# Performance work log

Measured on AMD Instinct MI355X. Metric: run time of the kernel, lower is better.

The kernel has to match this reference:

```python
import jax, jax.numpy as jnp
import numpy as np

WINDOW_SIZE = 11
C1 = 0.01 ** 2
C2 = 0.03 ** 2


def _make_window(size: int) -> jnp.ndarray:
    sigma = size / 6.0
    coords = jnp.arange(size, dtype=jnp.float32) - size // 2
    g = jnp.exp(-coords ** 2 / (2 * sigma ** 2))
    g = g / g.sum()
    w = jnp.outer(g, g)
    return w[None, None]  # [1,1,K,K]  (OIHW)


def _conv(x, w, pad):
    # x: [N,1,H,W], w: [1,1,K,K]
    return jax.lax.conv_general_dilated(
        x, w,
        window_strides=(1, 1),
        padding=[(pad, pad), (pad, pad)],
        dimension_numbers=("NCHW", "OIHW", "NCHW"),
    )


def setup_inputs() -> dict:
    key = jax.random.key(0)
    k1, k2 = jax.random.split(key)
    pred = jax.random.uniform(k1, (64, 1, 512, 512), dtype=jnp.float32)
    gt = jax.random.uniform(k2, (64, 1, 512, 512), dtype=jnp.float32)
    return {"pred": pred, "gt": gt}


def reference(pred, gt):
    w = _make_window(WINDOW_SIZE).astype(pred.dtype)
    pad = WINDOW_SIZE // 2
    mu1 = _conv(pred, w, pad)
    mu2 = _conv(gt, w, pad)
    sigma1 = _conv(pred * pred, w, pad) - mu1 ** 2
    sigma2 = _conv(gt * gt, w, pad) - mu2 ** 2
    sigma12 = _conv(pred * gt, w, pad) - mu1 * mu2
    ssim_map = (2 * mu1 * mu2 + C1) * (2 * sigma12 + C2) / (
        (mu1 ** 2 + mu2 ** 2 + C1) * (sigma1 + sigma2 + C2)
    )
    return 1 - ssim_map.mean()
```

## Files before the change

### kernel.cpp

```cpp
#include <hip/hip_runtime.h>
#include <math.h>

#define IMG_H 512
#define IMG_W 512
#define NIMG 64
#define TH 64
#define TCOLS 256
#define HALO 5
#define KSIZE 11
#define LROW (TCOLS + 2*HALO)

__global__ __launch_bounds__(256, 4)
void ssim_main(const float* __restrict__ pred, const float* __restrict__ gt,
               float* __restrict__ partial) {
    __shared__ float sp[2][LROW];
    __shared__ float sg[2][LROW];
    __shared__ float wsum[4];

    const int tid = threadIdx.x;
    const int bid = blockIdx.x;
    const int img = bid >> 4;
    const int rem = bid & 15;
    const int c0  = (rem & 1) * TCOLS;
    const int r0  = (rem >> 1) * TH;

    float wgt[KSIZE];
    {
        const float sigma = 11.0f / 6.0f;
        float s = 0.f;
        #pragma unroll
        for (int i = 0; i < KSIZE; ++i) {
            float d = (float)(i - 5);
            wgt[i] = expf(-d * d / (2.f * sigma * sigma));
            s += wgt[i];
        }
        float inv = 1.f / s;
        #pragma unroll
        for (int i = 0; i < KSIZE; ++i) wgt[i] *= inv;
    }

    const float* pimg = pred + (size_t)img * IMG_H * IMG_W;
    const float* gimg = gt   + (size_t)img * IMG_H * IMG_W;

    const int  cs0   = c0 - HALO + tid;
    const int  cs1   = cs0 + 256;
    const bool has2  = tid < (LROW - 256);
    const bool c0ok  = (cs0 >= 0) && (cs0 < IMG_W);
    const bool c1ok  = has2 && (cs1 < IMG_W);

    float stp0, stp1, stg0, stg1;

    auto load_row = [&](int r, float& p0, float& p1, float& g0, float& g1) {
        const bool rok = (r >= 0) && (r < IMG_H);
        const float* prow = pimg + (size_t)r * IMG_W;
        const float* grow = gimg + (size_t)r * IMG_W;
        p0 = (rok && c0ok) ? prow[cs0] : 0.f;
        g0 = (rok && c0ok) ? grow[cs0] : 0.f;
        p1 = (rok && c1ok) ? prow[cs1] : 0.f;
        g1 = (rok && c1ok) ? grow[cs1] : 0.f;
    };

    const int r_in0 = r0 - HALO;
    load_row(r_in0, stp0, stp1, stg0, stg1);

    float rp[KSIZE], rg[KSIZE], rpp[KSIZE], rgg[KSIZE], rpg[KSIZE];
    float lsum = 0.f;

    const float C1 = 1e-4f;
    const float C2 = 9e-4f;

    #pragma unroll 1
    for (int ob = 0; ob < 7; ++ob) {
        #pragma unroll
        for (int jj = 0; jj < KSIZE; ++jj) {
            const int i   = ob * KSIZE + jj;
            const int r   = r_in0 + i;
            const int cur = i & 1;

            sp[cur][tid] = stp0;
            sg[cur][tid] = stg0;
            if (has2) { sp[cur][tid + 256] = stp1; sg[cur][tid + 256] = stg1; }

            load_row(r + 1, stp0, stp1, stg0, stg1);

            __syncthreads();

            float hp = 0.f, hg = 0.f, hpp = 0.f, hgg = 0.f, hpg = 0.f;
            #pragma unroll
            for (int k = 0; k < KSIZE; ++k) {
                float p  = sp[cur][tid + k];
                float g  = sg[cur][tid + k];
                float t1 = wgt[k] * p;
                float t2 = wgt[k] * g;
                hp += t1;
                hg += t2;
                hpp = fmaf(t1, p, hpp);
                hgg = fmaf(t2, g, hgg);
                hpg = fmaf(t1, g, hpg);
            }
            rp[jj] = hp; rg[jj] = hg; rpp[jj] = hpp; rgg[jj] = hgg; rpg[jj] = hpg;

            if (i >= 10 && i < 10 + TH) {
                float mu1 = 0.f, mu2 = 0.f, svpp = 0.f, svgg = 0.f, svpg = 0.f;
                #pragma unroll
                for (int d = 0; d < KSIZE; ++d) {
                    const int slot = (jj + 1 + d) % KSIZE;
                    const float wv = wgt[d];
                    mu1  = fmaf(wv, rp[slot],  mu1);
                    mu2  = fmaf(wv, rg[slot],  mu2);
                    svpp = fmaf(wv, rpp[slot], svpp);
                    svgg = fmaf(wv, rgg[slot], svgg);
                    svpg = fmaf(wv, rpg[slot], svpg);
                }
                const float m11 = mu1 * mu1;
                const float m22 = mu2 * mu2;
                const float m12 = mu1 * mu2;
                const float s1  = svpp - m11;
                const float s2  = svgg - m22;
                const float s12 = svpg - m12;
                const float num = fmaf(2.f, m12, C1) * fmaf(2.f, s12, C2);
                const float den = (m11 + m22 + C1) * (s1 + s2 + C2);
                lsum += num * __builtin_amdgcn_rcpf(den);
            }
        }
    }

    #pragma unroll
    for (int off = 32; off > 0; off >>= 1) lsum += __shfl_down(lsum, off);
    if ((tid & 63) == 0) wsum[tid >> 6] = lsum;
    __syncthreads();
    if (tid == 0) {
        float b = wsum[0] + wsum[1] + wsum[2] + wsum[3];
        atomicAdd(partial, b);
    }
}

__global__ void ssim_final(const float* __restrict__ partial,
                           float* __restrict__ out) {
    out[0] = 1.f - partial[0] * (1.f / (float)((size_t)NIMG * IMG_H * IMG_W));
}

extern "C" void kernel_launch(void* const* d_in, const int* in_sizes, int n_in,
                              void* d_out, int out_size, void* d_ws, size_t ws_size,
                              hipStream_t stream) {
    const float* pred = (const float*)d_in[0];
    const float* gt   = (const float*)d_in[1];
    float* out = (float*)d_out;
    float* ws  = (float*)d_ws;

    hipMemsetAsync(ws, 0, sizeof(float), stream);

    const int nblocks = NIMG * (IMG_W / TCOLS) * (IMG_H / TH);
    ssim_main<<<nblocks, 256, 0, stream>>>(pred, gt, ws);
    ssim_final<<<1, 1, 0, stream>>>(ws, out);
}
```

Measured before the change: 191.5 us.

## Give each wavefront its own 64-column strip to replace block barriers with wave barriers

Each of the four wavefronts now processes an independent 64-column strip with its own single-buffered shared-memory row of 74 floats. The per-row __syncthreads is replaced by wave-local barriers, removing block-wide synchronisation. The row loop is unrolled through templated step calls. In exchange, each strip reloads its 10-column halo, raising halo overhead from 10/256 to 10/64 per row, and loads narrow to 64-wide segments. It also adds a clamp so rows past the tile's last needed input are not loaded.

Measured after the change: 185.3 us. -3.3%, faster.

```diff
diff --git a/kernel.cpp b/kernel.cpp
--- a/kernel.cpp
+++ b/kernel.cpp
@@ -1,28 +1,30 @@
 #include <hip/hip_runtime.h>
 #include <math.h>
+#include <type_traits>
 
 #define IMG_H 512
 #define IMG_W 512
 #define NIMG 64
 #define TH 64
-#define TCOLS 256
 #define HALO 5
 #define KSIZE 11
-#define LROW (TCOLS + 2*HALO)
+#define LROW 74
 
 __global__ __launch_bounds__(256, 4)
 void ssim_main(const float* __restrict__ pred, const float* __restrict__ gt,
                float* __restrict__ partial) {
-    __shared__ float sp[2][LROW];
-    __shared__ float sg[2][LROW];
+    __shared__ float sp[4][LROW];
+    __shared__ float sg[4][LROW];
     __shared__ float wsum[4];
 
-    const int tid = threadIdx.x;
-    const int bid = blockIdx.x;
-    const int img = bid >> 4;
-    const int rem = bid & 15;
-    const int c0  = (rem & 1) * TCOLS;
-    const int r0  = (rem >> 1) * TH;
+    const int tid  = threadIdx.x;
+    const int wv   = tid >> 6;
+    const int lane = tid & 63;
+    const int bid  = blockIdx.x;
+    const int img  = bid >> 4;
+    const int rem  = bid & 15;
+    const int c0   = (rem & 1) * 256 + wv * 64;
+    const int r0   = (rem >> 1) * TH;
 
     float wgt[KSIZE];
     {
@@ -42,92 +44,106 @@
     const float* pimg = pred + (size_t)img * IMG_H * IMG_W;
     const float* gimg = gt   + (size_t)img * IMG_H * IMG_W;
 
-    const int  cs0   = c0 - HALO + tid;
-    const int  cs1   = cs0 + 256;
-    const bool has2  = tid < (LROW - 256);
-    const bool c0ok  = (cs0 >= 0) && (cs0 < IMG_W);
-    const bool c1ok  = has2 && (cs1 < IMG_W);
+    const int  cs0  = c0 - HALO + lane;
+    const int  cs1  = cs0 + 64;
+    const bool has2 = lane < (LROW - 64);
+    const bool c0ok = (cs0 >= 0) && (cs0 < IMG_W);
+    const bool c1ok = has2 && (cs1 < IMG_W);
+    const int  r_in0 = r0 - HALO;
+    const int  rtop  = r_in0 + 73;
 
     float stp0, stp1, stg0, stg1;
-
-    auto load_row = [&](int r, float& p0, float& p1, float& g0, float& g1) {
-        const bool rok = (r >= 0) && (r < IMG_H);
-        const float* prow = pimg + (size_t)r * IMG_W;
-        const float* grow = gimg + (size_t)r * IMG_W;
-        p0 = (rok && c0ok) ? prow[cs0] : 0.f;
-        g0 = (rok && c0ok) ? grow[cs0] : 0.f;
-        p1 = (rok && c1ok) ? prow[cs1] : 0.f;
-        g1 = (rok && c1ok) ? grow[cs1] : 0.f;
+    auto load_row = [&](int rr) {
+        const bool rok = (rr >= 0) && (rr < IMG_H) && (rr <= rtop);
+        const float* prow = pimg + (size_t)rr * IMG_W;
+        const float* grow = gimg + (size_t)rr * IMG_W;
+        stp0 = (rok && c0ok) ? prow[cs0] : 0.f;
+        stg0 = (rok && c0ok) ? grow[cs0] : 0.f;
+        stp1 = (rok && c1ok) ? prow[cs1] : 0.f;
+        stg1 = (rok && c1ok) ? grow[cs1] : 0.f;
     };
-
-    const int r_in0 = r0 - HALO;
-    load_row(r_in0, stp0, stp1, stg0, stg1);
+    load_row(r_in0);
 
     float rp[KSIZE], rg[KSIZE], rpp[KSIZE], rgg[KSIZE], rpg[KSIZE];
     float lsum = 0.f;
+    const float C1v = 1e-4f;
+    const float C2v = 9e-4f;
 
-    const float C1 = 1e-4f;
-    const float C2 = 9e-4f;
+    float* swp = &sp[wv][0];
+    float* swg = &sg[wv][0];
+
+    auto step = [&](int i, auto jc) {
+        constexpr int jj = decltype(jc)::value;
+        const int r = r_in0 + i;
+
+        __builtin_amdgcn_wave_barrier();
+
+        swp[lane] = stp0;
+        swg[lane] = stg0;
+        if (has2) { swp[lane + 64] = stp1; swg[lane + 64] = stg1; }
+
+        load_row(r + 1);
+
+        __builtin_amdgcn_wave_barrier();
+
+        float hp = 0.f, hg = 0.f, hpp = 0.f, hgg = 0.f, hpg = 0.f;
+        #pragma unroll
+        for (int k = 0; k < KSIZE; ++k) {
+            float p  = swp[lane + k];
+            float g  = swg[lane + k];
+            float t1 = wgt[k] * p;
+            float t2 = wgt[k] * g;
+            hp += t1;
+            hg += t2;
+            hpp = fmaf(t1, p, hpp);
+            hgg = fmaf(t2, g, hgg);
+            hpg = fmaf(t1, g, hpg);
+        }
+        rp[jj] = hp; rg[jj] = hg; rpp[jj] = hpp; rgg[jj] = hgg; rpg[jj] = hpg;
+
+        if (i >= 10 && i < 10 + TH) {
+            float mu1 = 0.f, mu2 = 0.f, svpp = 0.f, svgg = 0.f, svpg = 0.f;
+            #pragma unroll
+            for (int d = 0; d < KSIZE; ++d) {
+                const int slot = (jj + 1 + d) % KSIZE;
+                const float wv2 = wgt[d];
+                mu1  = fmaf(wv2, rp[slot],  mu1);
+                mu2  = fmaf(wv2, rg[slot],  mu2);
+                svpp = fmaf(wv2, rpp[slot], svpp);
+                svgg = fmaf(wv2, rgg[slot], svgg);
+                svpg = fmaf(wv2, rpg[slot], svpg);
+            }
+            const float m11 = mu1 * mu1;
+            const float m22 = mu2 * mu2;
+            const float m12 = mu1 * mu2;
+            const float s1  = svpp - m11;
+            const float s2  = svgg - m22;
+            const float s12 = svpg - m12;
+            const float num = fmaf(2.f, m12, C1v) * fmaf(2.f, s12, C2v);
+            const float den = (m11 + m22 + C1v) * (s1 + s2 + C2v);
+            lsum += num * __builtin_amdgcn_rcpf(den);
+        }
+    };
 
     #pragma unroll 1
     for (int ob = 0; ob < 7; ++ob) {
-        #pragma unroll
-        for (int jj = 0; jj < KSIZE; ++jj) {
-            const int i   = ob * KSIZE + jj;
-            const int r   = r_in0 + i;
-            const int cur = i & 1;
-
-            sp[cur][tid] = stp0;
-            sg[cur][tid] = stg0;
-            if (has2) { sp[cur][tid + 256] = stp1; sg[cur][tid + 256] = stg1; }
-
-            load_row(r + 1, stp0, stp1, stg0, stg1);
-
-            __syncthreads();
-
-            float hp = 0.f, hg = 0.f, hpp = 0.f, hgg = 0.f, hpg = 0.f;
-            #pragma unroll
-            for (int k = 0; k < KSIZE; ++k) {
-                float p  = sp[cur][tid + k];
-                float g  = sg[cur][tid + k];
-                float t1 = wgt[k] * p;
-                float t2 = wgt[k] * g;
-                hp += t1;
-                hg += t2;
-                hpp = fmaf(t1, p, hpp);
-                hgg = fmaf(t2, g, hgg);
-                hpg = fmaf(t1, g, hpg);
-            }
-            rp[jj] = hp; rg[jj] = hg; rpp[jj] = hpp; rgg[jj] = hgg; rpg[jj] = hpg;
-
-            if (i >= 10 && i < 10 + TH) {
-                float mu1 = 0.f, mu2 = 0.f, svpp = 0.f, svgg = 0.f, svpg = 0.f;
-                #pragma unroll
-                for (int d = 0; d < KSIZE; ++d) {
-                    const int slot = (jj + 1 + d) % KSIZE;
-                    const float wv = wgt[d];
-                    mu1  = fmaf(wv, rp[slot],  mu1);
-                    mu2  = fmaf(wv, rg[slot],  mu2);
-                    svpp = fmaf(wv, rpp[slot], svpp);
-                    svgg = fmaf(wv, rgg[slot], svgg);
-                    svpg = fmaf(wv, rpg[slot], svpg);
-                }
-                const float m11 = mu1 * mu1;
-                const float m22 = mu2 * mu2;
-                const float m12 = mu1 * mu2;
-                const float s1  = svpp - m11;
-                const float s2  = svgg - m22;
-                const float s12 = svpg - m12;
-                const float num = fmaf(2.f, m12, C1) * fmaf(2.f, s12, C2);
-                const float den = (m11 + m22 + C1) * (s1 + s2 + C2);
-                lsum += num * __builtin_amdgcn_rcpf(den);
-            }
-        }
+        const int base = ob * KSIZE;
+        step(base + 0,  std::integral_constant<int, 0>{});
+        step(base + 1,  std::integral_constant<int, 1>{});
+        step(base + 2,  std::integral_constant<int, 2>{});
+        step(base + 3,  std::integral_constant<int, 3>{});
+        step(base + 4,  std::integral_constant<int, 4>{});
+        step(base + 5,  std::integral_constant<int, 5>{});
+        step(base + 6,  std::integral_constant<int, 6>{});
+        step(base + 7,  std::integral_constant<int, 7>{});
+        step(base + 8,  std::integral_constant<int, 8>{});
+        step(base + 9,  std::integral_constant<int, 9>{});
+        step(base + 10, std::integral_constant<int, 10>{});
     }
 
     #pragma unroll
     for (int off = 32; off > 0; off >>= 1) lsum += __shfl_down(lsum, off);
-    if ((tid & 63) == 0) wsum[tid >> 6] = lsum;
+    if (lane == 0) wsum[wv] = lsum;
     __syncthreads();
     if (tid == 0) {
         float b = wsum[0] + wsum[1] + wsum[2] + wsum[3];
@@ -150,7 +166,7 @@
 
     hipMemsetAsync(ws, 0, sizeof(float), stream);
 
-    const int nblocks = NIMG * (IMG_W / TCOLS) * (IMG_H / TH);
+    const int nblocks = NIMG * 16;
     ssim_main<<<nblocks, 256, 0, stream>>>(pred, gt, ws);
     ssim_final<<<1, 1, 0, stream>>>(ws, out);
 }
```
